# Performance work log

Measured on AMD Instinct MI355X. Metric: run time of the kernel, lower is better.

The kernel has to match this reference:

```python
import jax, jax.numpy as jnp
import numpy as np

R_EARTH = 6371.0


def haversine(coords):
    # coords: (B, N, 2) lat/lon in degrees -> (B, N, N) distances in km
    lat = jnp.deg2rad(coords[..., 0])
    lon = jnp.deg2rad(coords[..., 1])
    lat1, lon1 = lat[:, :, None], lon[:, :, None]   # (B,N,1)
    lat2, lon2 = lat[:, None, :], lon[:, None, :]   # (B,1,N)
    dlat, dlon = lat2 - lat1, lon2 - lon1
    a = jnp.sin(dlat / 2) ** 2 + jnp.cos(lat1) * jnp.cos(lat2) * jnp.sin(dlon / 2) ** 2
    a = jnp.clip(a, 0.0, 1.0)
    c = 2.0 * jnp.arctan2(jnp.sqrt(a), jnp.sqrt(1.0 - a))
    return R_EARTH * c


def setup_inputs() -> dict:
    key = jax.random.key(0)
    ks = jax.random.split(key, 16)
    B, N, T, D, H = 4, 256, 128, 512, 8
    hd = D // H
    s = 1.0 / np.sqrt(D)
    inp = {
        'x': jax.random.normal(ks[0], (B, N, T, D), dtype=jnp.float32),
        'coords': jax.random.uniform(ks[1], (B, N, 2), dtype=jnp.float32) * 90.0,
        'station_mask': jax.random.randint(ks[2], (B, N), 0, 2, dtype=jnp.int32),
        'Wq': jax.random.normal(ks[3], (D, D), dtype=jnp.float32) * s,
        'bq': jnp.zeros((D,), dtype=jnp.float32),
        'Wk': jax.random.normal(ks[4], (D, D), dtype=jnp.float32) * s,
        'bk': jnp.zeros((D,), dtype=jnp.float32),
        'Wv': jax.random.normal(ks[5], (D, D), dtype=jnp.float32) * s,
        'bv': jnp.zeros((D,), dtype=jnp.float32),
        'Wo': jax.random.normal(ks[6], (D, D), dtype=jnp.float32) * s,
        'bo': jnp.zeros((D,), dtype=jnp.float32),
        'Wd1': jax.random.normal(ks[7], (hd, 1), dtype=jnp.float32),
        'bd1': jnp.zeros((hd,), dtype=jnp.float32),
        'Wd2': jax.random.normal(ks[8], (H, hd), dtype=jnp.float32) / np.sqrt(hd),
        'bd2': jnp.zeros((H,), dtype=jnp.float32),
    }
    return inp


def reference(x, coords, station_mask, Wq, bq, Wk, bk, Wv, bv, Wo, bo, Wd1, bd1, Wd2, bd2):
    B, N, T, D = x.shape
    H = Wd2.shape[0]
    hd = D // H
    scale = jnp.sqrt(jnp.asarray(hd, dtype=x.dtype))

    x_repr = x.mean(axis=2)  # (B,N,D) temporal pooling

    def proj(W, b):
        y = x_repr @ W.T + b                       # (B,N,D)
        return y.reshape(B, N, H, hd).transpose(0, 2, 1, 3)  # (B,H,N,hd)

    Q, K, V = proj(Wq, bq), proj(Wk, bk), proj(Wv, bv)
    scores = jnp.einsum('bhnd,bhmd->bhnm', Q, K) / scale  # (B,H,N,N)

    # haversine distance -> 2-layer MLP bias, (B,N,N,H) -> (B,H,N,N)
    dist = haversine(coords)[..., None]                    # (B,N,N,1)
    hmid = jax.nn.relu(dist @ Wd1.T + bd1)                 # (B,N,N,hd)
    bias = (hmid @ Wd2.T + bd2).transpose(0, 3, 1, 2)      # (B,H,N,N)
    scores = scores + bias

    # mask invalid key stations
    scores = jnp.where(station_mask[:, None, None, :] == 0, -jnp.inf, scores)
    w = jax.nn.softmax(scores, axis=-1)

    out = jnp.einsum('bhnm,bhmd->bhnd', w, V)
    out = out.transpose(0, 2, 1, 3).reshape(B, N, D)
    out = out @ Wo.T + bo
    return jnp.broadcast_to(out[:, :, None, :], (B, N, T, D))
```

## Files before the change

### kernel.cpp

```cpp
#include <hip/hip_runtime.h>
#include <math.h>

#define Bc 4
#define Nc 256
#define Tc 128
#define Dc 512
#define Hc 8
#define HDc 64

typedef float f4v __attribute__((ext_vector_type(4)));

#define SWZ(row, k4) (((row) << 4) | ((k4) ^ (((row) >> 2) & 15)))

__global__ __launch_bounds__(256) void mean_kernel(const float* __restrict__ x,
                                                   float* __restrict__ xr) {
    const int bn = blockIdx.x;
    const int col = threadIdx.x & 127;
    const int half = threadIdx.x >> 7;
    const f4v* xp = (const f4v*)x + (size_t)bn * (Tc * Dc / 4)
                    + (size_t)(half * 64) * (Dc / 4) + col;
    f4v a[8];
#pragma unroll
    for (int u = 0; u < 8; ++u) a[u] = (f4v)(0.f);
    for (int t = 0; t < 64; t += 8) {
#pragma unroll
        for (int u = 0; u < 8; ++u)
            a[u] += __builtin_nontemporal_load(xp + (size_t)(t + u) * (Dc / 4));
    }
    f4v s = ((a[0] + a[1]) + (a[2] + a[3])) + ((a[4] + a[5]) + (a[6] + a[7]));
    __shared__ f4v red[256];
    red[threadIdx.x] = s;
    __syncthreads();
    if (threadIdx.x < 128) {
        f4v r = (red[threadIdx.x] + red[threadIdx.x + 128]) * (1.0f / Tc);
        ((f4v*)xr)[(size_t)bn * (Dc / 4) + threadIdx.x] = r;
    }
}

__device__ __forceinline__ void gemm_core(const float* __restrict__ A,
                                          const float* __restrict__ W,
                                          int i0, int j0, float acc[4][4]) {
    __shared__ float4 As4[1024];
    __shared__ float4 Ws4[1024];
    const int tid = threadIdx.x;
    const int ty = tid >> 4, tx = tid & 15;
    float4 pa[4], pw[4];
#pragma unroll
    for (int p = 0; p < 4; ++p) {
        pa[p] = *(const float4*)&A[(size_t)(i0 + p * 16 + ty) * Dc + tx * 4];
        pw[p] = *(const float4*)&W[(size_t)(j0 + p * 16 + ty) * Dc + tx * 4];
    }
    for (int kb = 0; kb < 8; ++kb) {
#pragma unroll
        for (int p = 0; p < 4; ++p) {
            As4[SWZ(p * 16 + ty, tx)] = pa[p];
            Ws4[SWZ(p * 16 + ty, tx)] = pw[p];
        }
        __syncthreads();
        if (kb < 7) {
            const int k0 = (kb + 1) * 64;
#pragma unroll
            for (int p = 0; p < 4; ++p) {
                pa[p] = *(const float4*)&A[(size_t)(i0 + p * 16 + ty) * Dc + k0 + tx * 4];
                pw[p] = *(const float4*)&W[(size_t)(j0 + p * 16 + ty) * Dc + k0 + tx * 4];
            }
        }
#pragma unroll
        for (int kk4 = 0; kk4 < 16; ++kk4) {
            float4 a[4], w[4];
#pragma unroll
            for (int q = 0; q < 4; ++q) a[q] = As4[SWZ(ty * 4 + q, kk4)];
#pragma unroll
            for (int c = 0; c < 4; ++c) w[c] = Ws4[SWZ(tx * 4 + c, kk4)];
#pragma unroll
            for (int q = 0; q < 4; ++q)
#pragma unroll
                for (int c = 0; c < 4; ++c) {
                    acc[q][c] += a[q].x * w[c].x;
                    acc[q][c] += a[q].y * w[c].y;
                    acc[q][c] += a[q].z * w[c].z;
                    acc[q][c] += a[q].w * w[c].w;
                }
        }
        __syncthreads();
    }
}

__global__ __launch_bounds__(256) void qkv_kernel(
    const float* __restrict__ xr, const float* __restrict__ Wq, const float* __restrict__ bq,
    const float* __restrict__ Wk, const float* __restrict__ bk,
    const float* __restrict__ Wv, const float* __restrict__ bv,
    float* __restrict__ Yq, float* __restrict__ Kt, float* __restrict__ Yv) {
    const int it = blockIdx.x;
    const int mat = blockIdx.y >> 3;
    const int jt = blockIdx.y & 7;
    const float* W = (mat == 0) ? Wq : (mat == 1) ? Wk : Wv;
    const float* bias = (mat == 0) ? bq : (mat == 1) ? bk : bv;
    const int i0 = it * 64, j0 = jt * 64;
    float acc[4][4] = {{0.f}};
    gemm_core(xr, W, i0, j0, acc);
    const int ty = threadIdx.x >> 4, tx = threadIdx.x & 15;
    if (mat == 1) {
        const int b = i0 >> 8;
        const int n0 = (i0 & 255) + ty * 4;
#pragma unroll
        for (int c = 0; c < 4; ++c) {
            const int j = j0 + tx * 4 + c;
            const float bj = bias[j];
            float4 v = make_float4(acc[0][c] + bj, acc[1][c] + bj,
                                   acc[2][c] + bj, acc[3][c] + bj);
            *(float4*)&Kt[(((size_t)b * Hc + jt) * HDc + (tx * 4 + c)) * Nc + n0] = v;
        }
    } else {
        float* Y = (mat == 0) ? Yq : Yv;
#pragma unroll
        for (int r = 0; r < 4; ++r) {
            const int i = i0 + ty * 4 + r;
            const int j = j0 + tx * 4;
            float4 o = make_float4(acc[r][0] + bias[j + 0], acc[r][1] + bias[j + 1],
                                   acc[r][2] + bias[j + 2], acc[r][3] + bias[j + 3]);
            *(float4*)&Y[(size_t)i * Dc + j] = o;
        }
    }
}

__global__ __launch_bounds__(256) void attn_kernel(
    const float* __restrict__ Yq, const float* __restrict__ Kt,
    const float* __restrict__ Yv, const float* __restrict__ coords,
    const int* __restrict__ mask, const float* __restrict__ Wd1,
    const float* __restrict__ bd1, const float* __restrict__ Wd2,
    const float* __restrict__ bd2, float* __restrict__ attnO) {
    const int bh = blockIdx.x >> 4;
    const int g = blockIdx.x & 15;
    const int b = bh >> 3, h = bh & 7;
    const int tid = threadIdx.x;
    const int wid = tid >> 6, lane = tid & 63;
    const int n_base = g * 16;
    const int q0 = wid * 4;

    __shared__ float sq[16][64];
    __shared__ float sw[16][256];
    __shared__ float slat[256], slon[256], scl[256];
    __shared__ __align__(16) float swd1[64];
    __shared__ __align__(16) float sbd1[64];
    __shared__ __align__(16) float swd2[64];
    __shared__ int smk[256];

    {
        const float DEG = 0.017453292519943295f;
        float la = coords[((size_t)b * Nc + tid) * 2 + 0] * DEG;
        float lo = coords[((size_t)b * Nc + tid) * 2 + 1] * DEG;
        slat[tid] = la; slon[tid] = lo; scl[tid] = __cosf(la);
        smk[tid] = mask[(size_t)b * Nc + tid];
        if (tid < 64) {
            swd1[tid] = Wd1[tid];
            sbd1[tid] = bd1[tid];
            swd2[tid] = Wd2[h * 64 + tid];
        }
#pragma unroll
        for (int r = 0; r < 4; ++r) {
            const int idx = r * 256 + tid;
            const int nl = idx >> 6, d = idx & 63;
            sq[nl][d] = Yq[((size_t)(b * Nc + n_base + nl)) * Dc + h * HDc + d] * 0.125f;
        }
    }
    __syncthreads();

    const float4* ktp = (const float4*)(Kt + (size_t)bh * HDc * Nc);
    f4v acc[4];
#pragma unroll
    for (int j = 0; j < 4; ++j) acc[j] = (f4v)(0.f);
#pragma unroll 8
    for (int k = 0; k < 64; ++k) {
        const float4 kv = ktp[k * 64 + lane];
        const f4v kvv = {kv.x, kv.y, kv.z, kv.w};
#pragma unroll
        for (int j = 0; j < 4; ++j) acc[j] += sq[q0 + j][k] * kvv;
    }

    const int mbase = lane * 4;
    float mlat[4], mlon[4], mcl[4];
    int mk[4];
#pragma unroll
    for (int jm = 0; jm < 4; ++jm) {
        mlat[jm] = slat[mbase + jm]; mlon[jm] = slon[mbase + jm];
        mcl[jm] = scl[mbase + jm];   mk[jm] = smk[mbase + jm];
    }
    float dist[4][4];
#pragma unroll
    for (int j = 0; j < 4; ++j) {
        const int n = n_base + q0 + j;
        const float lat1 = slat[n], lon1 = slon[n], cl1 = scl[n];
#pragma unroll
        for (int jm = 0; jm < 4; ++jm) {
            float sdlat = __sinf((mlat[jm] - lat1) * 0.5f);
            float sdlon = __sinf((mlon[jm] - lon1) * 0.5f);
            float a = sdlat * sdlat + cl1 * mcl[jm] * sdlon * sdlon;
            a = fminf(fmaxf(a, 0.f), 1.f);
            dist[j][jm] = 12742.0f * atan2f(sqrtf(a), sqrtf(1.0f - a));
        }
    }

    float bias[4][4];
#pragma unroll
    for (int j = 0; j < 4; ++j)
#pragma unroll
        for (int jm = 0; jm < 4; ++jm) bias[j][jm] = 0.f;
#pragma unroll 4
    for (int k4 = 0; k4 < 16; ++k4) {
        const float4 w1 = *(const float4*)&swd1[k4 * 4];
        const float4 b1 = *(const float4*)&sbd1[k4 * 4];
        const float4 w2 = *(const float4*)&swd2[k4 * 4];
#pragma unroll
        for (int j = 0; j < 4; ++j)
#pragma unroll
            for (int jm = 0; jm < 4; ++jm) {
                const float d = dist[j][jm];
                float bacc = bias[j][jm];
                bacc += fmaxf(d * w1.x + b1.x, 0.f) * w2.x;
                bacc += fmaxf(d * w1.y + b1.y, 0.f) * w2.y;
                bacc += fmaxf(d * w1.z + b1.z, 0.f) * w2.z;
                bacc += fmaxf(d * w1.w + b1.w, 0.f) * w2.w;
                bias[j][jm] = bacc;
            }
    }

    float inv[4];
    const float bd2h = bd2[h];
#pragma unroll
    for (int j = 0; j < 4; ++j) {
        float s[4];
#pragma unroll
        for (int jm = 0; jm < 4; ++jm) {
            s[jm] = acc[j][jm] + bias[j][jm] + bd2h;
            if (mk[jm] == 0) s[jm] = -1e30f;
        }
        float mx = fmaxf(fmaxf(s[0], s[1]), fmaxf(s[2], s[3]));
#pragma unroll
        for (int off = 32; off > 0; off >>= 1) mx = fmaxf(mx, __shfl_xor(mx, off, 64));
        float e0 = __expf(s[0] - mx), e1 = __expf(s[1] - mx);
        float e2 = __expf(s[2] - mx), e3 = __expf(s[3] - mx);
        ((float4*)sw[q0 + j])[lane] = make_float4(e0, e1, e2, e3);
        float sum = e0 + e1 + e2 + e3;
#pragma unroll
        for (int off = 32; off > 0; off >>= 1) sum += __shfl_xor(sum, off, 64);
        inv[j] = 1.0f / sum;
    }
    __syncthreads();

    const int mo = lane >> 4, d4 = lane & 15;
    const float* vbase = Yv + (size_t)b * Nc * Dc + h * HDc + d4 * 4;
    f4v o[4];
#pragma unroll
    for (int j = 0; j < 4; ++j) o[j] = (f4v)(0.f);
#pragma unroll 8
    for (int mq = 0; mq < 64; ++mq) {
        const int m = mq * 4 + mo;
        const f4v v = *(const f4v*)&vbase[(size_t)m * Dc];
#pragma unroll
        for (int j = 0; j < 4; ++j) o[j] += sw[q0 + j][m] * v;
    }
#pragma unroll
    for (int j = 0; j < 4; ++j) {
#pragma unroll
        for (int off = 16; off <= 32; off <<= 1) {
            o[j].x += __shfl_xor(o[j].x, off, 64);
            o[j].y += __shfl_xor(o[j].y, off, 64);
            o[j].z += __shfl_xor(o[j].z, off, 64);
            o[j].w += __shfl_xor(o[j].w, off, 64);
        }
        if (mo == 0) {
            const int n = n_base + q0 + j;
            f4v r = o[j] * inv[j];
            *(f4v*)&attnO[((size_t)(b * Nc + n)) * Dc + h * HDc + d4 * 4] = r;
        }
    }
}

__global__ __launch_bounds__(256) void oproj_bcast_kernel(
    const float* __restrict__ attnI, const float* __restrict__ Wo,
    const float* __restrict__ bo, float* __restrict__ out) {
    const int i0 = blockIdx.x * 64, j0 = blockIdx.y * 64;
    const int z = blockIdx.z;
    float acc[4][4] = {{0.f}};
    gemm_core(attnI, Wo, i0, j0, acc);

    __shared__ f4v tile[1024];
    const int ty = threadIdx.x >> 4, tx = threadIdx.x & 15;
#pragma unroll
    for (int q = 0; q < 4; ++q) {
        const int j = j0 + tx * 4;
        f4v v;
        v.x = acc[q][0] + bo[j + 0]; v.y = acc[q][1] + bo[j + 1];
        v.z = acc[q][2] + bo[j + 2]; v.w = acc[q][3] + bo[j + 3];
        tile[(ty * 4 + q) * 16 + tx] = v;
    }
    __syncthreads();

    const int d4 = threadIdx.x & 15;
    const int sub = threadIdx.x >> 4;
    for (int r = 0; r < 64; ++r) {
        const f4v val = tile[r * 16 + d4];
        float* rowbase = out + (size_t)(i0 + r) * Tc * Dc + j0;
#pragma unroll
        for (int tt = 0; tt < 4; ++tt) {
            const int t = z * 64 + tt * 16 + sub;
            __builtin_nontemporal_store(val, (f4v*)(rowbase + (size_t)t * Dc) + d4);
        }
    }
}

extern "C" void kernel_launch(void* const* d_in, const int* in_sizes, int n_in,
                              void* d_out, int out_size, void* d_ws, size_t ws_size,
                              hipStream_t stream) {
    const float* x      = (const float*)d_in[0];
    const float* coords = (const float*)d_in[1];
    const int*   smask  = (const int*)d_in[2];
    const float* Wq = (const float*)d_in[3];  const float* bq = (const float*)d_in[4];
    const float* Wk = (const float*)d_in[5];  const float* bk = (const float*)d_in[6];
    const float* Wv = (const float*)d_in[7];  const float* bv = (const float*)d_in[8];
    const float* Wo = (const float*)d_in[9];  const float* bo = (const float*)d_in[10];
    const float* Wd1 = (const float*)d_in[11]; const float* bd1 = (const float*)d_in[12];
    const float* Wd2 = (const float*)d_in[13]; const float* bd2 = (const float*)d_in[14];
    float* out = (float*)d_out;

    float* ws    = (float*)d_ws;
    const size_t BND = (size_t)Bc * Nc * Dc;
    float* xr    = ws;
    float* Yq    = xr + BND;
    float* Kt    = Yq + BND;
    float* Yv    = Kt + BND;
    float* attn  = Yv + BND;

    mean_kernel<<<Bc * Nc, 256, 0, stream>>>(x, xr);
    qkv_kernel<<<dim3(16, 24), 256, 0, stream>>>(xr, Wq, bq, Wk, bk, Wv, bv, Yq, Kt, Yv);
    attn_kernel<<<32 * 16, 256, 0, stream>>>(Yq, Kt, Yv, coords, smask,
                                             Wd1, bd1, Wd2, bd2, attn);
    oproj_bcast_kernel<<<dim3(16, 8, 2), 256, 0, stream>>>(attn, Wo, bo, out);
}
```

Measured before the change: 582.7 us.

## Fuse four pipeline stages into one cooperative persistent kernel with grid syncs

After: 750.0 us. 1.29x slower.

```diff
diff --git a/kernel.cpp b/kernel.cpp
--- a/kernel.cpp
+++ b/kernel.cpp
@@ -1,5 +1,8 @@
 #include <hip/hip_runtime.h>
+#include <hip/hip_cooperative_groups.h>
 #include <math.h>
+
+namespace cg = cooperative_groups;
 
 #define Bc 4
 #define Nc 256
@@ -8,9 +11,330 @@
 #define Hc 8
 #define HDc 64
 
+#define GRID_BLOCKS 512
+
 typedef float f4v __attribute__((ext_vector_type(4)));
 
 #define SWZ(row, k4) (((row) << 4) | ((k4) ^ (((row) >> 2) & 15)))
+
+struct AttnSmem {
+    float sq[16][64];
+    float sw[16][256];
+    float slat[256];
+    float slon[256];
+    float scl[256];
+    float swd1[64];
+    float sbd1[64];
+    float swd2[64];
+    int smk[256];
+};
+
+__device__ __forceinline__ void gemm_core(const float* __restrict__ A,
+                                          const float* __restrict__ W,
+                                          int i0, int j0, float acc[4][4],
+                                          float4* __restrict__ As4,
+                                          float4* __restrict__ Ws4) {
+    const int tid = threadIdx.x;
+    const int ty = tid >> 4, tx = tid & 15;
+    float4 pa[4], pw[4];
+#pragma unroll
+    for (int p = 0; p < 4; ++p) {
+        pa[p] = *(const float4*)&A[(size_t)(i0 + p * 16 + ty) * Dc + tx * 4];
+        pw[p] = *(const float4*)&W[(size_t)(j0 + p * 16 + ty) * Dc + tx * 4];
+    }
+    for (int kb = 0; kb < 8; ++kb) {
+#pragma unroll
+        for (int p = 0; p < 4; ++p) {
+            As4[SWZ(p * 16 + ty, tx)] = pa[p];
+            Ws4[SWZ(p * 16 + ty, tx)] = pw[p];
+        }
+        __syncthreads();
+        if (kb < 7) {
+            const int k0 = (kb + 1) * 64;
+#pragma unroll
+            for (int p = 0; p < 4; ++p) {
+                pa[p] = *(const float4*)&A[(size_t)(i0 + p * 16 + ty) * Dc + k0 + tx * 4];
+                pw[p] = *(const float4*)&W[(size_t)(j0 + p * 16 + ty) * Dc + k0 + tx * 4];
+            }
+        }
+#pragma unroll
+        for (int kk4 = 0; kk4 < 16; ++kk4) {
+            float4 a[4], w[4];
+#pragma unroll
+            for (int q = 0; q < 4; ++q) a[q] = As4[SWZ(ty * 4 + q, kk4)];
+#pragma unroll
+            for (int c = 0; c < 4; ++c) w[c] = Ws4[SWZ(tx * 4 + c, kk4)];
+#pragma unroll
+            for (int q = 0; q < 4; ++q)
+#pragma unroll
+                for (int c = 0; c < 4; ++c) {
+                    acc[q][c] += a[q].x * w[c].x;
+                    acc[q][c] += a[q].y * w[c].y;
+                    acc[q][c] += a[q].z * w[c].z;
+                    acc[q][c] += a[q].w * w[c].w;
+                }
+        }
+        __syncthreads();
+    }
+}
+
+__global__ __launch_bounds__(256) void fused_kernel(
+    const float* __restrict__ x, const float* __restrict__ coords,
+    const int* __restrict__ mask,
+    const float* __restrict__ Wq, const float* __restrict__ bq,
+    const float* __restrict__ Wk, const float* __restrict__ bk,
+    const float* __restrict__ Wv, const float* __restrict__ bv,
+    const float* __restrict__ Wo, const float* __restrict__ bo,
+    const float* __restrict__ Wd1, const float* __restrict__ bd1,
+    const float* __restrict__ Wd2, const float* __restrict__ bd2,
+    float* __restrict__ out,
+    float* __restrict__ xr, float* __restrict__ Yq, float* __restrict__ Kt,
+    float* __restrict__ Yv, float* __restrict__ attnO) {
+
+    __shared__ __align__(16) char smem_raw[32768];
+    cg::grid_group grid = cg::this_grid();
+    const int tid = threadIdx.x;
+
+    {
+        f4v* red = (f4v*)smem_raw;
+        const int col = tid & 127;
+        const int half = tid >> 7;
+#pragma unroll 1
+        for (int bn = blockIdx.x; bn < Bc * Nc; bn += GRID_BLOCKS) {
+            const f4v* xp = (const f4v*)x + (size_t)bn * (Tc * Dc / 4)
+                            + (size_t)(half * 64) * (Dc / 4) + col;
+            f4v a[8];
+#pragma unroll
+            for (int u = 0; u < 8; ++u) a[u] = (f4v)(0.f);
+            for (int t = 0; t < 64; t += 8) {
+#pragma unroll
+                for (int u = 0; u < 8; ++u)
+                    a[u] += __builtin_nontemporal_load(xp + (size_t)(t + u) * (Dc / 4));
+            }
+            f4v s = ((a[0] + a[1]) + (a[2] + a[3])) + ((a[4] + a[5]) + (a[6] + a[7]));
+            __syncthreads();
+            red[tid] = s;
+            __syncthreads();
+            if (tid < 128) {
+                f4v r = (red[tid] + red[tid + 128]) * (1.0f / Tc);
+                ((f4v*)xr)[(size_t)bn * (Dc / 4) + tid] = r;
+            }
+        }
+    }
+    grid.sync();
+
+    if (blockIdx.x < 384) {
+        const int it = blockIdx.x & 15;
+        const int ym = blockIdx.x >> 4;
+        const int mat = ym >> 3;
+        const int jt = ym & 7;
+        const float* W = (mat == 0) ? Wq : (mat == 1) ? Wk : Wv;
+        const float* bias = (mat == 0) ? bq : (mat == 1) ? bk : bv;
+        const int i0 = it * 64, j0 = jt * 64;
+        float acc[4][4] = {{0.f}};
+        float4* As4 = (float4*)smem_raw;
+        gemm_core(xr, W, i0, j0, acc, As4, As4 + 1024);
+        const int ty = tid >> 4, tx = tid & 15;
+        if (mat == 1) {
+            const int b = i0 >> 8;
+            const int n0 = (i0 & 255) + ty * 4;
+#pragma unroll
+            for (int c = 0; c < 4; ++c) {
+                const int j = j0 + tx * 4 + c;
+                const float bj = bias[j];
+                float4 v = make_float4(acc[0][c] + bj, acc[1][c] + bj,
+                                       acc[2][c] + bj, acc[3][c] + bj);
+                *(float4*)&Kt[(((size_t)b * Hc + jt) * HDc + (tx * 4 + c)) * Nc + n0] = v;
+            }
+        } else {
+            float* Y = (mat == 0) ? Yq : Yv;
+#pragma unroll
+            for (int r = 0; r < 4; ++r) {
+                const int i = i0 + ty * 4 + r;
+                const int j = j0 + tx * 4;
+                float4 o = make_float4(acc[r][0] + bias[j + 0], acc[r][1] + bias[j + 1],
+                                       acc[r][2] + bias[j + 2], acc[r][3] + bias[j + 3]);
+                *(float4*)&Y[(size_t)i * Dc + j] = o;
+            }
+        }
+    }
+    grid.sync();
+
+    {
+        AttnSmem& S = *(AttnSmem*)smem_raw;
+        const int bh = blockIdx.x >> 4;
+        const int g = blockIdx.x & 15;
+        const int b = bh >> 3, h = bh & 7;
+        const int wid = tid >> 6, lane = tid & 63;
+        const int n_base = g * 16;
+        const int q0 = wid * 4;
+
+        {
+            const float DEG = 0.017453292519943295f;
+            float la = coords[((size_t)b * Nc + tid) * 2 + 0] * DEG;
+            float lo = coords[((size_t)b * Nc + tid) * 2 + 1] * DEG;
+            S.slat[tid] = la; S.slon[tid] = lo; S.scl[tid] = __cosf(la);
+            S.smk[tid] = mask[(size_t)b * Nc + tid];
+            if (tid < 64) {
+                S.swd1[tid] = Wd1[tid];
+                S.sbd1[tid] = bd1[tid];
+                S.swd2[tid] = Wd2[h * 64 + tid];
+            }
+#pragma unroll
+            for (int r = 0; r < 4; ++r) {
+                const int idx = r * 256 + tid;
+                const int nl = idx >> 6, d = idx & 63;
+                S.sq[nl][d] = Yq[((size_t)(b * Nc + n_base + nl)) * Dc + h * HDc + d] * 0.125f;
+            }
+        }
+        __syncthreads();
+
+        const float4* ktp = (const float4*)(Kt + (size_t)bh * HDc * Nc);
+        f4v acc[4];
+#pragma unroll
+        for (int j = 0; j < 4; ++j) acc[j] = (f4v)(0.f);
+#pragma unroll 8
+        for (int k = 0; k < 64; ++k) {
+            const float4 kv = ktp[k * 64 + lane];
+            const f4v kvv = {kv.x, kv.y, kv.z, kv.w};
+#pragma unroll
+            for (int j = 0; j < 4; ++j) acc[j] += S.sq[q0 + j][k] * kvv;
+        }
+
+        const int mbase = lane * 4;
+        float mlat[4], mlon[4], mcl[4];
+        int mk[4];
+#pragma unroll
+        for (int jm = 0; jm < 4; ++jm) {
+            mlat[jm] = S.slat[mbase + jm]; mlon[jm] = S.slon[mbase + jm];
+            mcl[jm] = S.scl[mbase + jm];   mk[jm] = S.smk[mbase + jm];
+        }
+        float dist[4][4];
+#pragma unroll
+        for (int j = 0; j < 4; ++j) {
+            const int n = n_base + q0 + j;
+            const float lat1 = S.slat[n], lon1 = S.slon[n], cl1 = S.scl[n];
+#pragma unroll
+            for (int jm = 0; jm < 4; ++jm) {
+                float sdlat = __sinf((mlat[jm] - lat1) * 0.5f);
+                float sdlon = __sinf((mlon[jm] - lon1) * 0.5f);
+                float a = sdlat * sdlat + cl1 * mcl[jm] * sdlon * sdlon;
+                a = fminf(fmaxf(a, 0.f), 1.f);
+                dist[j][jm] = 12742.0f * atan2f(sqrtf(a), sqrtf(1.0f - a));
+            }
+        }
+
+        float bias[4][4];
+#pragma unroll
+        for (int j = 0; j < 4; ++j)
+#pragma unroll
+            for (int jm = 0; jm < 4; ++jm) bias[j][jm] = 0.f;
+#pragma unroll 4
+        for (int k4 = 0; k4 < 16; ++k4) {
+            const float4 w1 = *(const float4*)&S.swd1[k4 * 4];
+            const float4 b1 = *(const float4*)&S.sbd1[k4 * 4];
+            const float4 w2 = *(const float4*)&S.swd2[k4 * 4];
+#pragma unroll
+            for (int j = 0; j < 4; ++j)
+#pragma unroll
+                for (int jm = 0; jm < 4; ++jm) {
+                    const float d = dist[j][jm];
+                    float bacc = bias[j][jm];
+                    bacc += fmaxf(d * w1.x + b1.x, 0.f) * w2.x;
+                    bacc += fmaxf(d * w1.y + b1.y, 0.f) * w2.y;
+                    bacc += fmaxf(d * w1.z + b1.z, 0.f) * w2.z;
+                    bacc += fmaxf(d * w1.w + b1.w, 0.f) * w2.w;
+                    bias[j][jm] = bacc;
+                }
+        }
+
+        float inv[4];
+        const float bd2h = bd2[h];
+#pragma unroll
+        for (int j = 0; j < 4; ++j) {
+            float s[4];
+#pragma unroll
+            for (int jm = 0; jm < 4; ++jm) {
+                s[jm] = acc[j][jm] + bias[j][jm] + bd2h;
+                if (mk[jm] == 0) s[jm] = -1e30f;
+            }
+            float mx = fmaxf(fmaxf(s[0], s[1]), fmaxf(s[2], s[3]));
+#pragma unroll
+            for (int off = 32; off > 0; off >>= 1) mx = fmaxf(mx, __shfl_xor(mx, off, 64));
+            float e0 = __expf(s[0] - mx), e1 = __expf(s[1] - mx);
+            float e2 = __expf(s[2] - mx), e3 = __expf(s[3] - mx);
+            ((float4*)S.sw[q0 + j])[lane] = make_float4(e0, e1, e2, e3);
+            float sum = e0 + e1 + e2 + e3;
+#pragma unroll
+            for (int off = 32; off > 0; off >>= 1) sum += __shfl_xor(sum, off, 64);
+            inv[j] = 1.0f / sum;
+        }
+        __syncthreads();
+
+        const int mo = lane >> 4, d4 = lane & 15;
+        const float* vbase = Yv + (size_t)b * Nc * Dc + h * HDc + d4 * 4;
+        f4v o[4];
+#pragma unroll
+        for (int j = 0; j < 4; ++j) o[j] = (f4v)(0.f);
+#pragma unroll 8
+        for (int mq = 0; mq < 64; ++mq) {
+            const int m = mq * 4 + mo;
+            const f4v v = *(const f4v*)&vbase[(size_t)m * Dc];
+#pragma unroll
+            for (int j = 0; j < 4; ++j) o[j] += S.sw[q0 + j][m] * v;
+        }
+#pragma unroll
+        for (int j = 0; j < 4; ++j) {
+#pragma unroll
+            for (int off = 16; off <= 32; off <<= 1) {
+                o[j].x += __shfl_xor(o[j].x, off, 64);
+                o[j].y += __shfl_xor(o[j].y, off, 64);
+                o[j].z += __shfl_xor(o[j].z, off, 64);
+                o[j].w += __shfl_xor(o[j].w, off, 64);
+            }
+            if (mo == 0) {
+                const int n = n_base + q0 + j;
+                f4v r = o[j] * inv[j];
+                *(f4v*)&attnO[((size_t)(b * Nc + n)) * Dc + h * HDc + d4 * 4] = r;
+            }
+        }
+    }
+    grid.sync();
+
+    if (blockIdx.x < 256) {
+        const int u = blockIdx.x;
+        const int i0 = (u & 15) * 64;
+        const int j0 = ((u >> 4) & 7) * 64;
+        const int z = u >> 7;
+        float acc[4][4] = {{0.f}};
+        float4* As4 = (float4*)smem_raw;
+        gemm_core(attnO, Wo, i0, j0, acc, As4, As4 + 1024);
+
+        f4v* tile = (f4v*)smem_raw;
+        const int ty = tid >> 4, tx = tid & 15;
+#pragma unroll
+        for (int q = 0; q < 4; ++q) {
+            const int j = j0 + tx * 4;
+            f4v v;
+            v.x = acc[q][0] + bo[j + 0]; v.y = acc[q][1] + bo[j + 1];
+            v.z = acc[q][2] + bo[j + 2]; v.w = acc[q][3] + bo[j + 3];
+            tile[(ty * 4 + q) * 16 + tx] = v;
+        }
+        __syncthreads();
+
+        const int d4 = tid & 15;
+        const int sub = tid >> 4;
+        for (int r = 0; r < 64; ++r) {
+            const f4v val = tile[r * 16 + d4];
+            float* rowbase = out + (size_t)(i0 + r) * Tc * Dc + j0;
+#pragma unroll
+            for (int tt = 0; tt < 4; ++tt) {
+                const int t = z * 64 + tt * 16 + sub;
+                __builtin_nontemporal_store(val, (f4v*)(rowbase + (size_t)t * Dc) + d4);
+            }
+        }
+    }
+}
 
 __global__ __launch_bounds__(256) void mean_kernel(const float* __restrict__ x,
                                                    float* __restrict__ xr) {
@@ -37,60 +361,13 @@
     }
 }
 
-__device__ __forceinline__ void gemm_core(const float* __restrict__ A,
-                                          const float* __restrict__ W,
-                                          int i0, int j0, float acc[4][4]) {
-    __shared__ float4 As4[1024];
-    __shared__ float4 Ws4[1024];
-    const int tid = threadIdx.x;
-    const int ty = tid >> 4, tx = tid & 15;
-    float4 pa[4], pw[4];
-#pragma unroll
-    for (int p = 0; p < 4; ++p) {
-        pa[p] = *(const float4*)&A[(size_t)(i0 + p * 16 + ty) * Dc + tx * 4];
-        pw[p] = *(const float4*)&W[(size_t)(j0 + p * 16 + ty) * Dc + tx * 4];
-    }
-    for (int kb = 0; kb < 8; ++kb) {
-#pragma unroll
-        for (int p = 0; p < 4; ++p) {
-            As4[SWZ(p * 16 + ty, tx)] = pa[p];
-            Ws4[SWZ(p * 16 + ty, tx)] = pw[p];
-        }
-        __syncthreads();
-        if (kb < 7) {
-            const int k0 = (kb + 1) * 64;
-#pragma unroll
-            for (int p = 0; p < 4; ++p) {
-                pa[p] = *(const float4*)&A[(size_t)(i0 + p * 16 + ty) * Dc + k0 + tx * 4];
-                pw[p] = *(const float4*)&W[(size_t)(j0 + p * 16 + ty) * Dc + k0 + tx * 4];
-            }
-        }
-#pragma unroll
-        for (int kk4 = 0; kk4 < 16; ++kk4) {
-            float4 a[4], w[4];
-#pragma unroll
-            for (int q = 0; q < 4; ++q) a[q] = As4[SWZ(ty * 4 + q, kk4)];
-#pragma unroll
-            for (int c = 0; c < 4; ++c) w[c] = Ws4[SWZ(tx * 4 + c, kk4)];
-#pragma unroll
-            for (int q = 0; q < 4; ++q)
-#pragma unroll
-                for (int c = 0; c < 4; ++c) {
-                    acc[q][c] += a[q].x * w[c].x;
-                    acc[q][c] += a[q].y * w[c].y;
-                    acc[q][c] += a[q].z * w[c].z;
-                    acc[q][c] += a[q].w * w[c].w;
-                }
-        }
-        __syncthreads();
-    }
-}
-
 __global__ __launch_bounds__(256) void qkv_kernel(
     const float* __restrict__ xr, const float* __restrict__ Wq, const float* __restrict__ bq,
     const float* __restrict__ Wk, const float* __restrict__ bk,
     const float* __restrict__ Wv, const float* __restrict__ bv,
     float* __restrict__ Yq, float* __restrict__ Kt, float* __restrict__ Yv) {
+    __shared__ float4 As4[1024];
+    __shared__ float4 Ws4[1024];
     const int it = blockIdx.x;
     const int mat = blockIdx.y >> 3;
     const int jt = blockIdx.y & 7;
@@ -98,7 +375,7 @@
     const float* bias = (mat == 0) ? bq : (mat == 1) ? bk : bv;
     const int i0 = it * 64, j0 = jt * 64;
     float acc[4][4] = {{0.f}};
-    gemm_core(xr, W, i0, j0, acc);
+    gemm_core(xr, W, i0, j0, acc, As4, Ws4);
     const int ty = threadIdx.x >> 4, tx = threadIdx.x & 15;
     if (mat == 1) {
         const int b = i0 >> 8;
@@ -138,30 +415,24 @@
     const int n_base = g * 16;
     const int q0 = wid * 4;
 
-    __shared__ float sq[16][64];
-    __shared__ float sw[16][256];
-    __shared__ float slat[256], slon[256], scl[256];
-    __shared__ __align__(16) float swd1[64];
-    __shared__ __align__(16) float sbd1[64];
-    __shared__ __align__(16) float swd2[64];
-    __shared__ int smk[256];
+    __shared__ AttnSmem S;
 
     {
         const float DEG = 0.017453292519943295f;
         float la = coords[((size_t)b * Nc + tid) * 2 + 0] * DEG;
         float lo = coords[((size_t)b * Nc + tid) * 2 + 1] * DEG;
-        slat[tid] = la; slon[tid] = lo; scl[tid] = __cosf(la);
-        smk[tid] = mask[(size_t)b * Nc + tid];
+        S.slat[tid] = la; S.slon[tid] = lo; S.scl[tid] = __cosf(la);
+        S.smk[tid] = mask[(size_t)b * Nc + tid];
         if (tid < 64) {
-            swd1[tid] = Wd1[tid];
-            sbd1[tid] = bd1[tid];
-            swd2[tid] = Wd2[h * 64 + tid];
+            S.swd1[tid] = Wd1[tid];
+            S.sbd1[tid] = bd1[tid];
+            S.swd2[tid] = Wd2[h * 64 + tid];
         }
 #pragma unroll
         for (int r = 0; r < 4; ++r) {
             const int idx = r * 256 + tid;
             const int nl = idx >> 6, d = idx & 63;
-            sq[nl][d] = Yq[((size_t)(b * Nc + n_base + nl)) * Dc + h * HDc + d] * 0.125f;
+            S.sq[nl][d] = Yq[((size_t)(b * Nc + n_base + nl)) * Dc + h * HDc + d] * 0.125f;
         }
     }
     __syncthreads();
@@ -175,7 +446,7 @@
         const float4 kv = ktp[k * 64 + lane];
         const f4v kvv = {kv.x, kv.y, kv.z, kv.w};
 #pragma unroll
-        for (int j = 0; j < 4; ++j) acc[j] += sq[q0 + j][k] * kvv;
+        for (int j = 0; j < 4; ++j) acc[j] += S.sq[q0 + j][k] * kvv;
     }
 
     const int mbase = lane * 4;
@@ -183,14 +454,14 @@
     int mk[4];
 #pragma unroll
     for (int jm = 0; jm < 4; ++jm) {
-        mlat[jm] = slat[mbase + jm]; mlon[jm] = slon[mbase + jm];
-        mcl[jm] = scl[mbase + jm];   mk[jm] = smk[mbase + jm];
+        mlat[jm] = S.slat[mbase + jm]; mlon[jm] = S.slon[mbase + jm];
+        mcl[jm] = S.scl[mbase + jm];   mk[jm] = S.smk[mbase + jm];
     }
     float dist[4][4];
 #pragma unroll
     for (int j = 0; j < 4; ++j) {
         const int n = n_base + q0 + j;
-        const float lat1 = slat[n], lon1 = slon[n], cl1 = scl[n];
+        const float lat1 = S.slat[n], lon1 = S.slon[n], cl1 = S.scl[n];
 #pragma unroll
         for (int jm = 0; jm < 4; ++jm) {
             float sdlat = __sinf((mlat[jm] - lat1) * 0.5f);
@@ -208,9 +479,9 @@
         for (int jm = 0; jm < 4; ++jm) bias[j][jm] = 0.f;
 #pragma unroll 4
     for (int k4 = 0; k4 < 16; ++k4) {
-        const float4 w1 = *(const float4*)&swd1[k4 * 4];
-        const float4 b1 = *(const float4*)&sbd1[k4 * 4];
-        const float4 w2 = *(const float4*)&swd2[k4 * 4];
+        const float4 w1 = *(const float4*)&S.swd1[k4 * 4];
+        const float4 b1 = *(const float4*)&S.sbd1[k4 * 4];
+        const float4 w2 = *(const float4*)&S.swd2[k4 * 4];
 #pragma unroll
         for (int j = 0; j < 4; ++j)
 #pragma unroll
@@ -240,7 +511,7 @@
         for (int off = 32; off > 0; off >>= 1) mx = fmaxf(mx, __shfl_xor(mx, off, 64));
         float e0 = __expf(s[0] - mx), e1 = __expf(s[1] - mx);
         float e2 = __expf(s[2] - mx), e3 = __expf(s[3] - mx);
-        ((float4*)sw[q0 + j])[lane] = make_float4(e0, e1, e2, e3);
+        ((float4*)S.sw[q0 + j])[lane] = make_float4(e0, e1, e2, e3);
         float sum = e0 + e1 + e2 + e3;
 #pragma unroll
         for (int off = 32; off > 0; off >>= 1) sum += __shfl_xor(sum, off, 64);
@@ -258,7 +529,7 @@
         const int m = mq * 4 + mo;
         const f4v v = *(const f4v*)&vbase[(size_t)m * Dc];
 #pragma unroll
-        for (int j = 0; j < 4; ++j) o[j] += sw[q0 + j][m] * v;
+        for (int j = 0; j < 4; ++j) o[j] += S.sw[q0 + j][m] * v;
     }
 #pragma unroll
     for (int j = 0; j < 4; ++j) {
@@ -280,10 +551,12 @@
 __global__ __launch_bounds__(256) void oproj_bcast_kernel(
     const float* __restrict__ attnI, const float* __restrict__ Wo,
     const float* __restrict__ bo, float* __restrict__ out) {
+    __shared__ float4 As4[1024];
+    __shared__ float4 Ws4[1024];
     const int i0 = blockIdx.x * 64, j0 = blockIdx.y * 64;
     const int z = blockIdx.z;
     float acc[4][4] = {{0.f}};
-    gemm_core(attnI, Wo, i0, j0, acc);
+    gemm_core(attnI, Wo, i0, j0, acc, As4, Ws4);
 
     __shared__ f4v tile[1024];
     const int ty = threadIdx.x >> 4, tx = threadIdx.x & 15;
@@ -332,9 +605,20 @@
     float* Yv    = Kt + BND;
     float* attn  = Yv + BND;
 
-    mean_kernel<<<Bc * Nc, 256, 0, stream>>>(x, xr);
-    qkv_kernel<<<dim3(16, 24), 256, 0, stream>>>(xr, Wq, bq, Wk, bk, Wv, bv, Yq, Kt, Yv);
-    attn_kernel<<<32 * 16, 256, 0, stream>>>(Yq, Kt, Yv, coords, smask,
-                                             Wd1, bd1, Wd2, bd2, attn);
-    oproj_bcast_kernel<<<dim3(16, 8, 2), 256, 0, stream>>>(attn, Wo, bo, out);
+    void* args[] = {(void*)&x, (void*)&coords, (void*)&smask,
+                    (void*)&Wq, (void*)&bq, (void*)&Wk, (void*)&bk,
+                    (void*)&Wv, (void*)&bv, (void*)&Wo, (void*)&bo,
+                    (void*)&Wd1, (void*)&bd1, (void*)&Wd2, (void*)&bd2,
+                    (void*)&out,
+                    (void*)&xr, (void*)&Yq, (void*)&Kt, (void*)&Yv, (void*)&attn};
+    hipError_t err = hipLaunchCooperativeKernel((const void*)fused_kernel,
+                                                dim3(GRID_BLOCKS), dim3(256),
+                                                args, 0, stream);
+    if (err != hipSuccess) {
+        mean_kernel<<<Bc * Nc, 256, 0, stream>>>(x, xr);
+        qkv_kernel<<<dim3(16, 24), 256, 0, stream>>>(xr, Wq, bq, Wk, bk, Wv, bv, Yq, Kt, Yv);
+        attn_kernel<<<32 * 16, 256, 0, stream>>>(Yq, Kt, Yv, coords, smask,
+                                                 Wd1, bd1, Wd2, bd2, attn);
+        oproj_bcast_kernel<<<dim3(16, 8, 2), 256, 0, stream>>>(attn, Wo, bo, out);
+    }
 }
```

## Fuse attention with output projection and broadcast store per station group

Applied to the files above, without the earlier changes.

After: 585.9 us. About the same (+0.5%).

```diff
diff --git a/kernel.cpp b/kernel.cpp
--- a/kernel.cpp
+++ b/kernel.cpp
@@ -13,7 +13,9 @@
 #define SWZ(row, k4) (((row) << 4) | ((k4) ^ (((row) >> 2) & 15)))
 
 __global__ __launch_bounds__(256) void mean_kernel(const float* __restrict__ x,
-                                                   float* __restrict__ xr) {
+                                                   float* __restrict__ xr,
+                                                   const float* __restrict__ Wo,
+                                                   float* __restrict__ WoT) {
     const int bn = blockIdx.x;
     const int col = threadIdx.x & 127;
     const int half = threadIdx.x >> 7;
@@ -34,6 +36,20 @@
     if (threadIdx.x < 128) {
         f4v r = (red[threadIdx.x] + red[threadIdx.x + 128]) * (1.0f / Tc);
         ((f4v*)xr)[(size_t)bn * (Dc / 4) + threadIdx.x] = r;
+    }
+    if (bn < 16) {
+        const int r0 = bn * 32;
+#pragma unroll 4
+        for (int u = 0; u < 16; ++u) {
+            const int job = u * 256 + threadIdx.x;
+            const int r = job >> 7;
+            const int k4 = job & 127;
+            const float4 v = *(const float4*)&Wo[(size_t)(r0 + r) * Dc + k4 * 4];
+            WoT[(size_t)(k4 * 4 + 0) * Dc + r0 + r] = v.x;
+            WoT[(size_t)(k4 * 4 + 1) * Dc + r0 + r] = v.y;
+            WoT[(size_t)(k4 * 4 + 2) * Dc + r0 + r] = v.z;
+            WoT[(size_t)(k4 * 4 + 3) * Dc + r0 + r] = v.w;
+        }
     }
 }
 
@@ -124,49 +140,52 @@
     }
 }
 
-__global__ __launch_bounds__(256) void attn_kernel(
+__global__ __launch_bounds__(512) void attn_oproj_kernel(
     const float* __restrict__ Yq, const float* __restrict__ Kt,
     const float* __restrict__ Yv, const float* __restrict__ coords,
     const int* __restrict__ mask, const float* __restrict__ Wd1,
     const float* __restrict__ bd1, const float* __restrict__ Wd2,
-    const float* __restrict__ bd2, float* __restrict__ attnO) {
-    const int bh = blockIdx.x >> 4;
-    const int g = blockIdx.x & 15;
-    const int b = bh >> 3, h = bh & 7;
+    const float* __restrict__ bd2, const float* __restrict__ WoT,
+    const float* __restrict__ bo, float* __restrict__ out) {
+    const int b = blockIdx.x >> 6;
+    const int n4 = (blockIdx.x & 63) * 4;
     const int tid = threadIdx.x;
     const int wid = tid >> 6, lane = tid & 63;
-    const int n_base = g * 16;
-    const int q0 = wid * 4;
-
-    __shared__ float sq[16][64];
-    __shared__ float sw[16][256];
+    const int h = wid;
+
+    __shared__ __align__(16) float sqf[4][512];
+    __shared__ __align__(16) float sw[8][4][256];
+    __shared__ __align__(16) float sO[4][512];
+    __shared__ __align__(16) float sOut[4][512];
     __shared__ float slat[256], slon[256], scl[256];
     __shared__ __align__(16) float swd1[64];
     __shared__ __align__(16) float sbd1[64];
-    __shared__ __align__(16) float swd2[64];
+    __shared__ __align__(16) float swd2[512];
     __shared__ int smk[256];
 
     {
         const float DEG = 0.017453292519943295f;
-        float la = coords[((size_t)b * Nc + tid) * 2 + 0] * DEG;
-        float lo = coords[((size_t)b * Nc + tid) * 2 + 1] * DEG;
-        slat[tid] = la; slon[tid] = lo; scl[tid] = __cosf(la);
-        smk[tid] = mask[(size_t)b * Nc + tid];
+        if (tid < 256) {
+            float la = coords[((size_t)b * Nc + tid) * 2 + 0] * DEG;
+            float lo = coords[((size_t)b * Nc + tid) * 2 + 1] * DEG;
+            slat[tid] = la; slon[tid] = lo; scl[tid] = __cosf(la);
+            smk[tid] = mask[(size_t)b * Nc + tid];
+        }
         if (tid < 64) {
             swd1[tid] = Wd1[tid];
             sbd1[tid] = bd1[tid];
-            swd2[tid] = Wd2[h * 64 + tid];
-        }
-#pragma unroll
-        for (int r = 0; r < 4; ++r) {
-            const int idx = r * 256 + tid;
-            const int nl = idx >> 6, d = idx & 63;
-            sq[nl][d] = Yq[((size_t)(b * Nc + n_base + nl)) * Dc + h * HDc + d] * 0.125f;
-        }
+        }
+        swd2[tid] = Wd2[tid];
+        const int row = tid >> 7, c4 = tid & 127;
+        const float4 qv = *(const float4*)&Yq[((size_t)(b * Nc + n4 + row)) * Dc + c4 * 4];
+        sqf[row][c4 * 4 + 0] = qv.x * 0.125f;
+        sqf[row][c4 * 4 + 1] = qv.y * 0.125f;
+        sqf[row][c4 * 4 + 2] = qv.z * 0.125f;
+        sqf[row][c4 * 4 + 3] = qv.w * 0.125f;
     }
     __syncthreads();
 
-    const float4* ktp = (const float4*)(Kt + (size_t)bh * HDc * Nc);
+    const float4* ktp = (const float4*)(Kt + ((size_t)(b * Hc + h)) * HDc * Nc);
     f4v acc[4];
 #pragma unroll
     for (int j = 0; j < 4; ++j) acc[j] = (f4v)(0.f);
@@ -175,7 +194,7 @@
         const float4 kv = ktp[k * 64 + lane];
         const f4v kvv = {kv.x, kv.y, kv.z, kv.w};
 #pragma unroll
-        for (int j = 0; j < 4; ++j) acc[j] += sq[q0 + j][k] * kvv;
+        for (int j = 0; j < 4; ++j) acc[j] += sqf[j][h * HDc + k] * kvv;
     }
 
     const int mbase = lane * 4;
@@ -189,7 +208,7 @@
     float dist[4][4];
 #pragma unroll
     for (int j = 0; j < 4; ++j) {
-        const int n = n_base + q0 + j;
+        const int n = n4 + j;
         const float lat1 = slat[n], lon1 = slon[n], cl1 = scl[n];
 #pragma unroll
         for (int jm = 0; jm < 4; ++jm) {
@@ -210,7 +229,7 @@
     for (int k4 = 0; k4 < 16; ++k4) {
         const float4 w1 = *(const float4*)&swd1[k4 * 4];
         const float4 b1 = *(const float4*)&sbd1[k4 * 4];
-        const float4 w2 = *(const float4*)&swd2[k4 * 4];
+        const float4 w2 = *(const float4*)&swd2[h * HDc + k4 * 4];
 #pragma unroll
         for (int j = 0; j < 4; ++j)
 #pragma unroll
@@ -240,13 +259,12 @@
         for (int off = 32; off > 0; off >>= 1) mx = fmaxf(mx, __shfl_xor(mx, off, 64));
         float e0 = __expf(s[0] - mx), e1 = __expf(s[1] - mx);
         float e2 = __expf(s[2] - mx), e3 = __expf(s[3] - mx);
-        ((float4*)sw[q0 + j])[lane] = make_float4(e0, e1, e2, e3);
+        ((float4*)sw[h][j])[lane] = make_float4(e0, e1, e2, e3);
         float sum = e0 + e1 + e2 + e3;
 #pragma unroll
         for (int off = 32; off > 0; off >>= 1) sum += __shfl_xor(sum, off, 64);
         inv[j] = 1.0f / sum;
     }
-    __syncthreads();
 
     const int mo = lane >> 4, d4 = lane & 15;
     const float* vbase = Yv + (size_t)b * Nc * Dc + h * HDc + d4 * 4;
@@ -258,7 +276,7 @@
         const int m = mq * 4 + mo;
         const f4v v = *(const f4v*)&vbase[(size_t)m * Dc];
 #pragma unroll
-        for (int j = 0; j < 4; ++j) o[j] += sw[q0 + j][m] * v;
+        for (int j = 0; j < 4; ++j) o[j] += sw[h][j][m] * v;
     }
 #pragma unroll
     for (int j = 0; j < 4; ++j) {
@@ -270,42 +288,50 @@
             o[j].w += __shfl_xor(o[j].w, off, 64);
         }
         if (mo == 0) {
-            const int n = n_base + q0 + j;
             f4v r = o[j] * inv[j];
-            *(f4v*)&attnO[((size_t)(b * Nc + n)) * Dc + h * HDc + d4 * 4] = r;
-        }
-    }
-}
-
-__global__ __launch_bounds__(256) void oproj_bcast_kernel(
-    const float* __restrict__ attnI, const float* __restrict__ Wo,
-    const float* __restrict__ bo, float* __restrict__ out) {
-    const int i0 = blockIdx.x * 64, j0 = blockIdx.y * 64;
-    const int z = blockIdx.z;
-    float acc[4][4] = {{0.f}};
-    gemm_core(attnI, Wo, i0, j0, acc);
-
-    __shared__ f4v tile[1024];
-    const int ty = threadIdx.x >> 4, tx = threadIdx.x & 15;
-#pragma unroll
-    for (int q = 0; q < 4; ++q) {
-        const int j = j0 + tx * 4;
-        f4v v;
-        v.x = acc[q][0] + bo[j + 0]; v.y = acc[q][1] + bo[j + 1];
-        v.z = acc[q][2] + bo[j + 2]; v.w = acc[q][3] + bo[j + 3];
-        tile[(ty * 4 + q) * 16 + tx] = v;
+            *(f4v*)&sO[j][h * HDc + d4 * 4] = r;
+        }
     }
     __syncthreads();
 
-    const int d4 = threadIdx.x & 15;
-    const int sub = threadIdx.x >> 4;
-    for (int r = 0; r < 64; ++r) {
-        const f4v val = tile[r * 16 + d4];
-        float* rowbase = out + (size_t)(i0 + r) * Tc * Dc + j0;
-#pragma unroll
-        for (int tt = 0; tt < 4; ++tt) {
-            const int t = z * 64 + tt * 16 + sub;
-            __builtin_nontemporal_store(val, (f4v*)(rowbase + (size_t)t * Dc) + d4);
+    {
+        const int jj = tid;
+        float a0 = 0.f, a1 = 0.f, a2 = 0.f, a3 = 0.f;
+#pragma unroll 4
+        for (int k4 = 0; k4 < 128; ++k4) {
+            const float4 q0 = *(const float4*)&sO[0][k4 * 4];
+            const float4 q1 = *(const float4*)&sO[1][k4 * 4];
+            const float4 q2 = *(const float4*)&sO[2][k4 * 4];
+            const float4 q3 = *(const float4*)&sO[3][k4 * 4];
+            const float w0 = WoT[(size_t)(k4 * 4 + 0) * Dc + jj];
+            const float w1 = WoT[(size_t)(k4 * 4 + 1) * Dc + jj];
+            const float w2 = WoT[(size_t)(k4 * 4 + 2) * Dc + jj];
+            const float w3 = WoT[(size_t)(k4 * 4 + 3) * Dc + jj];
+            a0 += q0.x * w0; a0 += q0.y * w1; a0 += q0.z * w2; a0 += q0.w * w3;
+            a1 += q1.x * w0; a1 += q1.y * w1; a1 += q1.z * w2; a1 += q1.w * w3;
+            a2 += q2.x * w0; a2 += q2.y * w1; a2 += q2.z * w2; a2 += q2.w * w3;
+            a3 += q3.x * w0; a3 += q3.y * w1; a3 += q3.z * w2; a3 += q3.w * w3;
+        }
+        const float bj = bo[jj];
+        sOut[0][jj] = a0 + bj;
+        sOut[1][jj] = a1 + bj;
+        sOut[2][jj] = a2 + bj;
+        sOut[3][jj] = a3 + bj;
+    }
+    __syncthreads();
+
+    {
+        const int c0 = tid & 127;
+        const int tg = tid >> 7;
+#pragma unroll
+        for (int q = 0; q < 4; ++q) {
+            const f4v val = *(const f4v*)&sOut[q][c0 * 4];
+            f4v* rb = (f4v*)(out + (((size_t)(b * Nc + n4 + q)) * Tc + tg * 32) * Dc) + c0;
+#pragma unroll 8
+            for (int tt = 0; tt < 32; ++tt) {
+                __builtin_nontemporal_store(val, rb);
+                rb += Dc / 4;
+            }
         }
     }
 }
@@ -330,11 +356,10 @@
     float* Yq    = xr + BND;
     float* Kt    = Yq + BND;
     float* Yv    = Kt + BND;
-    float* attn  = Yv + BND;
-
-    mean_kernel<<<Bc * Nc, 256, 0, stream>>>(x, xr);
+    float* WoT   = Yv + BND;
+
+    mean_kernel<<<Bc * Nc, 256, 0, stream>>>(x, xr, Wo, WoT);
     qkv_kernel<<<dim3(16, 24), 256, 0, stream>>>(xr, Wq, bq, Wk, bk, Wv, bv, Yq, Kt, Yv);
-    attn_kernel<<<32 * 16, 256, 0, stream>>>(Yq, Kt, Yv, coords, smask,
-                                             Wd1, bd1, Wd2, bd2, attn);
-    oproj_bcast_kernel<<<dim3(16, 8, 2), 256, 0, stream>>>(attn, Wo, bo, out);
-}
+    attn_oproj_kernel<<<Bc * 64, 512, 0, stream>>>(Yq, Kt, Yv, coords, smask,
+                                                   Wd1, bd1, Wd2, bd2, WoT, bo, out);
+}
```
